# Optimization experiments

Measured on AMD Instinct MI355X. Metric: run time of the kernel, lower is better.

## Reference

```python
import jax, jax.numpy as jnp
import numpy as np

EPS = 1e-5
GROUPS = 32


def conv1x1(x, W, b):
    # x: (B,C,T), W: (O,C), b: (O,)
    return jnp.einsum('bct,oc->bot', x, W) + b[None, :, None]


def group_norm(x, gamma, beta):
    B, C, T = x.shape
    xg = x.reshape(B, GROUPS, (C // GROUPS) * T)
    mu = xg.mean(axis=-1, keepdims=True)
    var = xg.var(axis=-1, keepdims=True)
    xn = ((xg - mu) * jax.lax.rsqrt(var + EPS)).reshape(B, C, T)
    return xn * gamma[None, :, None] + beta[None, :, None]


def block(x, W, b, gamma, beta):
    return jax.nn.relu(group_norm(conv1x1(x, W, b), gamma, beta))


def setup_inputs() -> dict:
    key = jax.random.key(0)
    ks = jax.random.split(key, 8)
    B, C, P, T, TF = 4, 512, 512, 2048, 4096
    inp = {
        'feature': jax.random.normal(ks[0], (B, C, T), jnp.float32),
        'frame_level_feature': jax.random.uniform(ks[1], (B, C, TF), jnp.float32),
        # cur_point_conv: conv1x1 C->P + GN(32,P)
        'W1': jax.random.normal(ks[2], (P, C), jnp.float32) / np.sqrt(C),
        'b1': jnp.zeros((P,), jnp.float32),
        'g1': jnp.ones((P,), jnp.float32),
        'be1': jnp.zeros((P,), jnp.float32),
        # lr_conv: conv1x1 C->2P + GN(32,2P)
        'W2': jax.random.normal(ks[3], (2 * P, C), jnp.float32) / np.sqrt(C),
        'b2': jnp.zeros((2 * P,), jnp.float32),
        'g2': jnp.ones((2 * P,), jnp.float32),
        'be2': jnp.zeros((2 * P,), jnp.float32),
        # proposal_conv: conv1x1 4P->C + GN(32,C)
        'W3': jax.random.normal(ks[4], (C, 4 * P), jnp.float32) / np.sqrt(4 * P),
        'b3': jnp.zeros((C,), jnp.float32),
        'g3': jnp.ones((C,), jnp.float32),
        'be3': jnp.zeros((C,), jnp.float32),
    }
    return inp


def reference(feature, frame_level_feature, W1, b1, g1, be1, W2, b2, g2, be2, W3, b3, g3, be3):
    fm_short = block(feature, W1, b1, g1, be1)          # (B,P,T)
    feat = block(feature, W2, b2, g2, be2)              # (B,2P,T)
    t = feature.shape[2]
    # inverse-CDF resampling (uses batch 0 statistics, as original)
    mean_values = frame_level_feature.mean(axis=1)[0]   # (TF,)
    mean_values = mean_values / mean_values.sum()
    cdf = (jnp.cumsum(mean_values) * t).astype(jnp.int32)
    cdf = jnp.minimum(cdf, t - 1)                       # (TF,)
    # exact vectorization of findNearNum loop: first index with minimal |cdf-i|
    targets = jnp.arange(t, dtype=jnp.int32)
    idx = jnp.argmin(jnp.abs(cdf[None, :] - targets[:, None]), axis=1)  # (t,)
    sampled = frame_level_feature[:, :, idx]            # (B,C,t)
    mixed = jnp.concatenate([sampled, feat, fm_short], axis=1)  # (B,4P,t)
    mixed = block(mixed, W3, b3, g3, be3)               # (B,C,t)
    return (mixed, feat)
```

## Files before the change

### kernel.cpp

```cpp
#include <hip/hip_runtime.h>

typedef unsigned short u16;
typedef unsigned int   u32;
typedef __attribute__((ext_vector_type(8))) short short8;
typedef __attribute__((ext_vector_type(4))) float f32x4;

__device__ __forceinline__ float bf2f(u16 v) {
  return __uint_as_float(((u32)v) << 16);
}
__device__ __forceinline__ u16 f2bf(float f) {
  u32 u = __float_as_uint(f);
  u32 r = (u + 0x7FFFu + ((u >> 16) & 1u)) >> 16;
  return (u16)r;
}
__device__ __forceinline__ float relu(float x) { return x < 0.f ? 0.f : x; }

__device__ __forceinline__ void gld16(const void* g, void* l) {
  __builtin_amdgcn_global_load_lds((const __attribute__((address_space(1))) u32*)g,
                                   (__attribute__((address_space(3))) u32*)l, 16, 0, 0);
}

__global__ void colmean_part_kernel(const float* __restrict__ frame,
                                    double* __restrict__ partD) {
  int tf = blockIdx.x * 256 + threadIdx.x;
  int ch = blockIdx.y;
  const float* f0 = frame + tf + (size_t)ch * 64 * 4096;
  double s = 0.0;
  for (int c = 0; c < 64; ++c) s += (double)f0[(size_t)c * 4096];
  partD[ch * 4096 + tf] = s;
}

__global__ void scanD_kernel(const double* __restrict__ partD, int* __restrict__ cdf) {
  __shared__ double part[256];
  __shared__ double base[256];
  __shared__ double Ss;
  int tid = threadIdx.x;
  double loc[16];
  double s = 0.0;
#pragma unroll
  for (int i = 0; i < 16; ++i) {
    int tf = tid * 16 + i;
    double m = 0.0;
#pragma unroll
    for (int ch = 0; ch < 8; ++ch) m += partD[ch * 4096 + tf];
    loc[i] = m / 512.0;
    s += loc[i];
  }
  part[tid] = s;
  __syncthreads();
  if (tid == 0) {
    double t = 0.0;
    for (int i = 0; i < 256; ++i) t += part[i];
    Ss = t;
  }
  __syncthreads();
  double S = Ss;
  s = 0.0;
#pragma unroll
  for (int i = 0; i < 16; ++i) { loc[i] = loc[i] / S; s += loc[i]; }
  part[tid] = s;
  __syncthreads();
  if (tid == 0) {
    double c = 0.0;
    for (int i = 0; i < 256; ++i) { base[i] = c; c += part[i]; }
  }
  __syncthreads();
  double c = base[tid];
#pragma unroll
  for (int i = 0; i < 16; ++i) {
    c += loc[i];
    int iv = (int)(c * 2048.0);
    cdf[tid * 16 + i] = iv < 2047 ? iv : 2047;
  }
}

__global__ void argmin_kernel(const int* __restrict__ cdf, int* __restrict__ idx) {
  __shared__ int sd[256], sj[256];
  int target = blockIdx.x;
  int tid = threadIdx.x;
  int best = 0x7fffffff, bj = 0x7fffffff;
  for (int j = tid; j < 4096; j += 256) {
    int d = cdf[j] - target; d = d < 0 ? -d : d;
    if (d < best) { best = d; bj = j; }
  }
  sd[tid] = best; sj[tid] = bj;
  __syncthreads();
  for (int s = 128; s > 0; s >>= 1) {
    if (tid < s) {
      if (sd[tid+s] < sd[tid] || (sd[tid+s] == sd[tid] && sj[tid+s] < sj[tid])) {
        sd[tid] = sd[tid+s]; sj[tid] = sj[tid+s];
      }
    }
    __syncthreads();
  }
  if (tid == 0) idx[target] = sj[0];
}

__global__ void gatherT_kernel(const float* __restrict__ frame, const int* __restrict__ idx,
                               u16* __restrict__ X3T) {
  __shared__ u16 tile[64][65];
  __shared__ int sidx[64];
  int cb = blockIdx.x * 64, t0 = blockIdx.y * 64, b = blockIdx.z;
  int tid = threadIdx.x;
  if (tid < 64) {
    int it = idx[t0 + tid];
    sidx[tid] = it < 0 ? 0 : (it > 4095 ? 4095 : it);
  }
  __syncthreads();
  const float* fb = frame + (size_t)b * 512 * 4096;
  for (int i = tid; i < 4096; i += 256) {
    int r = i >> 6, tt = i & 63;
    tile[tt][r] = f2bf(fb[(size_t)(cb + r) * 4096 + sidx[tt]]);
  }
  __syncthreads();
  u16* xb = X3T + (size_t)b * 2048 * 2048;
  for (int i = tid; i < 4096; i += 256) {
    int r = i >> 6, cc = i & 63;
    xb[(size_t)(t0 + r) * 2048 + cb + cc] = tile[r][cc];
  }
}

__global__ void transposeCT_kernel(const float* __restrict__ X, u16* __restrict__ XT) {
  __shared__ u16 tile[64][65];
  int cb = blockIdx.x * 64, t0 = blockIdx.y * 64, b = blockIdx.z;
  int tid = threadIdx.x;
  const float* xb = X + (size_t)b * 512 * 2048;
  for (int i = tid; i < 4096; i += 256) {
    int r = i >> 6, tt = i & 63;
    tile[tt][r] = f2bf(xb[(size_t)(cb + r) * 2048 + t0 + tt]);
  }
  __syncthreads();
  u16* xtb = XT + (size_t)b * 2048 * 512;
  for (int i = tid; i < 4096; i += 256) {
    int r = i >> 6, cc = i & 63;
    xtb[(size_t)(t0 + r) * 512 + cb + cc] = tile[r][cc];
  }
}

__global__ void convW12_kernel(const float* __restrict__ W1, const float* __restrict__ W2,
                               u16* __restrict__ dst) {
  int i = blockIdx.x * 256 + threadIdx.x;
  dst[i] = f2bf(i < 262144 ? W1[i] : W2[i - 262144]);
}
__global__ void convW_kernel(const float* __restrict__ src, u16* __restrict__ dst, int n) {
  int i = blockIdx.x * 256 + threadIdx.x;
  if (i < n) dst[i] = f2bf(src[i]);
}

__global__ __launch_bounds__(128) void gemm12_kernel(
    const u16* __restrict__ A, const u16* __restrict__ Bt,
    const float* __restrict__ b1, const float* __restrict__ b2,
    float* __restrict__ Y)
{
  const int K = 512;
  __shared__ short As[2][2048];
  __shared__ short Bs[2][4096];
  const int tid = threadIdx.x;
  const int lane = tid & 63;
  const int w = tid >> 6;
  const int nt = blockIdx.x, mt = blockIdx.y, bb = blockIdx.z;
  const u16* Ab = A + (size_t)mt * 64 * K;
  const u16* Bb = Bt + ((size_t)bb * 2048 + (size_t)nt * 128) * K;
  const int lm = lane & 15, lq = lane >> 4;
  f32x4 acc[4][4] = {};

  auto stage = [&](int buf, int kt) {
#pragma unroll
    for (int p = 0; p < 2; ++p) {
      int chunk = tid + 128 * p;
      int row = chunk >> 2, ko = (chunk & 3) << 3;
      gld16(Ab + (size_t)row * K + kt + ko, (char*)As[buf] + chunk * 16);
    }
#pragma unroll
    for (int p = 0; p < 4; ++p) {
      int chunk = tid + 128 * p;
      int row = chunk >> 2, ko = (chunk & 3) << 3;
      gld16(Bb + (size_t)row * K + kt + ko, (char*)Bs[buf] + chunk * 16);
    }
  };

  stage(0, 0);
  for (int s = 0; s < 16; ++s) {
    int cur = s & 1;
    __syncthreads();
    if (s + 1 < 16) stage(cur ^ 1, (s + 1) << 5);
    short8 af[4], bfv[4];
#pragma unroll
    for (int i = 0; i < 4; ++i)
      af[i] = *(const short8*)(As[cur] + ((i * 16 + lm) * 32 + lq * 8));
#pragma unroll
    for (int j = 0; j < 4; ++j)
      bfv[j] = *(const short8*)(Bs[cur] + ((w * 64 + j * 16 + lm) * 32 + lq * 8));
#pragma unroll
    for (int i = 0; i < 4; ++i)
#pragma unroll
      for (int j = 0; j < 4; ++j)
        acc[i][j] = __builtin_amdgcn_mfma_f32_16x16x32_bf16(af[i], bfv[j], acc[i][j], 0, 0, 0);
  }
#pragma unroll
  for (int i = 0; i < 4; ++i) {
    int mbase = mt * 64 + i * 16 + lq * 4;
#pragma unroll
    for (int e = 0; e < 4; ++e) {
      int m = mbase + e;
      float bv = m < 512 ? b1[m] : b2[m - 512];
      float* yp = Y + ((size_t)bb * 1536 + m) * 2048 + nt * 128 + w * 64 + lm;
#pragma unroll
      for (int j = 0; j < 4; ++j)
        yp[j * 16] = acc[i][j][e] + bv;
    }
  }
}

__global__ __launch_bounds__(128) void gemm3s_kernel(
    const u16* __restrict__ A, const u16* __restrict__ Bt,
    const float* __restrict__ bias, float* __restrict__ Yp)
{
  const int K = 2048;
  __shared__ short As[2][2048];
  __shared__ short Bs[2][4096];
  const int tid = threadIdx.x;
  const int lane = tid & 63;
  const int w = tid >> 6;
  const int nt = blockIdx.x, mt = blockIdx.y;
  const int bb = blockIdx.z >> 1, ks = blockIdx.z & 1;
  const u16* Ab = A + (size_t)mt * 64 * K + ks * 1024;
  const u16* Bb = Bt + ((size_t)bb * 2048 + (size_t)nt * 128) * K + ks * 1024;
  const int lm = lane & 15, lq = lane >> 4;
  f32x4 acc[4][4] = {};

  auto stage = [&](int buf, int kt) {
#pragma unroll
    for (int p = 0; p < 2; ++p) {
      int chunk = tid + 128 * p;
      int row = chunk >> 2, ko = (chunk & 3) << 3;
      gld16(Ab + (size_t)row * K + kt + ko, (char*)As[buf] + chunk * 16);
    }
#pragma unroll
    for (int p = 0; p < 4; ++p) {
      int chunk = tid + 128 * p;
      int row = chunk >> 2, ko = (chunk & 3) << 3;
      gld16(Bb + (size_t)row * K + kt + ko, (char*)Bs[buf] + chunk * 16);
    }
  };

  stage(0, 0);
  for (int s = 0; s < 32; ++s) {
    int cur = s & 1;
    __syncthreads();
    if (s + 1 < 32) stage(cur ^ 1, (s + 1) << 5);
    short8 af[4], bfv[4];
#pragma unroll
    for (int i = 0; i < 4; ++i)
      af[i] = *(const short8*)(As[cur] + ((i * 16 + lm) * 32 + lq * 8));
#pragma unroll
    for (int j = 0; j < 4; ++j)
      bfv[j] = *(const short8*)(Bs[cur] + ((w * 64 + j * 16 + lm) * 32 + lq * 8));
#pragma unroll
    for (int i = 0; i < 4; ++i)
#pragma unroll
      for (int j = 0; j < 4; ++j)
        acc[i][j] = __builtin_amdgcn_mfma_f32_16x16x32_bf16(af[i], bfv[j], acc[i][j], 0, 0, 0);
  }
#pragma unroll
  for (int i = 0; i < 4; ++i) {
    int mbase = mt * 64 + i * 16 + lq * 4;
#pragma unroll
    for (int e = 0; e < 4; ++e) {
      int m = mbase + e;
      float bv = ks ? 0.f : bias[m];
      float* yp = Yp + ((size_t)(ks * 4 + bb) * 512 + m) * 2048 + nt * 128 + w * 64 + lm;
#pragma unroll
      for (int j = 0; j < 4; ++j)
        yp[j * 16] = acc[i][j][e] + bv;
    }
  }
}

__global__ void statsP12_kernel(const float* __restrict__ Y12,
                                float* __restrict__ raw1, float* __restrict__ raw2) {
  int chunk = blockIdx.x, gy = blockIdx.y, b = blockIdx.z, tid = threadIdx.x;
  int cpg, chBase, g; float* raw;
  if (gy < 32) { if (chunk >= 8) return; cpg = 16; chBase = 0;   g = gy;      raw = raw1; }
  else         {                         cpg = 32; chBase = 512; g = gy - 32; raw = raw2; }
  const float* base = Y12 + ((size_t)b * 1536 + chBase + g * cpg) * 2048 + (size_t)chunk * 4096;
  float s = 0.f, ss = 0.f;
#pragma unroll
  for (int i = 0; i < 16; ++i) { float v = base[tid + 256 * i]; s += v; ss += v * v; }
  __shared__ float s1[256], s2[256];
  s1[tid] = s; s2[tid] = ss;
  __syncthreads();
  for (int st = 128; st > 0; st >>= 1) {
    if (tid < st) { s1[tid] += s1[tid + st]; s2[tid] += s2[tid + st]; }
    __syncthreads();
  }
  if (tid == 0) {
    atomicAdd(&raw[(b * 32 + g) * 2],     s1[0]);
    atomicAdd(&raw[(b * 32 + g) * 2 + 1], s2[0]);
  }
}

__global__ void stats3p_kernel(const float* __restrict__ Yp, float* __restrict__ raw) {
  int chunk = blockIdx.x, g = blockIdx.y, b = blockIdx.z, tid = threadIdx.x;
  const float* base = Yp + ((size_t)b * 512 + g * 16) * 2048 + (size_t)chunk * 4096;
  float s = 0.f, ss = 0.f;
#pragma unroll
  for (int i = 0; i < 16; ++i) {
    int o = tid + 256 * i;
    float v = base[o] + base[o + 4194304];
    s += v; ss += v * v;
  }
  __shared__ float s1[256], s2[256];
  s1[tid] = s; s2[tid] = ss;
  __syncthreads();
  for (int st = 128; st > 0; st >>= 1) {
    if (tid < st) { s1[tid] += s1[tid + st]; s2[tid] += s2[tid + st]; }
    __syncthreads();
  }
  if (tid == 0) {
    atomicAdd(&raw[(b * 32 + g) * 2],     s1[0]);
    atomicAdd(&raw[(b * 32 + g) * 2 + 1], s2[0]);
  }
}

__global__ void statsFin12_kernel(const float* __restrict__ raw1, const float* __restrict__ raw2,
                                  float* __restrict__ st1, float* __restrict__ st2) {
  int i = threadIdx.x;
  const float* raw = i < 128 ? raw1 : raw2;
  float* st = i < 128 ? st1 : st2;
  int j = i & 127;
  float n = i < 128 ? 32768.f : 65536.f;
  float mu = raw[j * 2] / n;
  float var = raw[j * 2 + 1] / n - mu * mu;
  st[j * 2] = mu;
  st[j * 2 + 1] = 1.0f / sqrtf(var + 1e-5f);
}
__global__ void statsFin_kernel(const float* __restrict__ raw, float* __restrict__ stats,
                                float n) {
  int i = threadIdx.x;
  float mu = raw[i * 2] / n;
  float var = raw[i * 2 + 1] / n - mu * mu;
  stats[i * 2] = mu;
  stats[i * 2 + 1] = 1.0f / sqrtf(var + 1e-5f);
}

__global__ void normT_kernel(const float* __restrict__ Y, const float* __restrict__ stats,
                             const float* __restrict__ gamma, const float* __restrict__ beta,
                             int rowsB, int chBase, int C, int gShift,
                             u16* __restrict__ X3T, int colBase,
                             float* __restrict__ featOut) {
  __shared__ u16 tile[64][65];
  int b = blockIdx.z, c0 = blockIdx.y * 64, t0 = blockIdx.x * 64;
  const float* yb = Y + ((size_t)b * rowsB + chBase) * 2048;
  for (int i = threadIdx.x; i < 4096; i += 256) {
    int r = i >> 6, cc = i & 63;
    int ch = c0 + r;
    int gI = (b * 32 + (ch >> gShift)) * 2;
    float mu = stats[gI], rs = stats[gI + 1];
    float v = yb[(size_t)ch * 2048 + t0 + cc];
    float o = relu((v - mu) * rs * gamma[ch] + beta[ch]);
    tile[cc][r] = f2bf(o);
    if (featOut) featOut[((size_t)b * C + ch) * 2048 + t0 + cc] = o;
  }
  __syncthreads();
  for (int i = threadIdx.x; i < 4096; i += 256) {
    int r = i >> 6, cc = i & 63;
    X3T[((size_t)b * 2048 + t0 + r) * 2048 + colBase + c0 + cc] = tile[r][cc];
  }
}

__global__ void norm3_kernel(const float* __restrict__ Yp, const float* __restrict__ stats,
                             const float* __restrict__ gamma, const float* __restrict__ beta,
                             float* __restrict__ out) {
  int i = blockIdx.x * 256 + threadIdx.x;
  int b = i >> 20;
  int ch = (i >> 11) & 511;
  int gI = (b * 32 + (ch >> 4)) * 2;
  float mu = stats[gI], rs = stats[gI + 1];
  float v = Yp[i] + Yp[i + 4194304];
  out[i] = relu((v - mu) * rs * gamma[ch] + beta[ch]);
}

extern "C" void kernel_launch(void* const* d_in, const int* in_sizes, int n_in,
                              void* d_out, int out_size, void* d_ws, size_t ws_size,
                              hipStream_t stream) {
  const float* feature = (const float*)d_in[0];
  const float* frame   = (const float*)d_in[1];
  const float* W1 = (const float*)d_in[2];
  const float* b1 = (const float*)d_in[3];
  const float* g1 = (const float*)d_in[4];
  const float* be1 = (const float*)d_in[5];
  const float* W2 = (const float*)d_in[6];
  const float* b2 = (const float*)d_in[7];
  const float* g2 = (const float*)d_in[8];
  const float* be2 = (const float*)d_in[9];
  const float* W3 = (const float*)d_in[10];
  const float* b3 = (const float*)d_in[11];
  const float* g3 = (const float*)d_in[12];
  const float* be3 = (const float*)d_in[13];

  char* ws = (char*)d_ws;
  u16*    X3T   = (u16*)(ws + 0);
  float*  Y12f  = (float*)(ws + 33554432);
  float*  Y3p   = (float*)(ws + 33554432);
  u16*    W3b   = (u16*)(ws + 67108864);
  double* partD = (double*)(ws + 50331648);
  u16*    featT = (u16*)(ws + 83886080);
  u16*    W12b  = (u16*)(ws + 92274688);
  int*    cdf   = (int*)(ws + 93847552);
  int*    idx   = (int*)(ws + 93863936);
  float*  raw1  = (float*)(ws + 93872128);
  float*  raw2  = (float*)(ws + 93873152);
  float*  raw3  = (float*)(ws + 93874176);
  float*  st1   = (float*)(ws + 93875200);
  float*  st2   = (float*)(ws + 93876224);
  float*  st3   = (float*)(ws + 93877248);

  float* outMixed = (float*)d_out;
  float* outFeat  = outMixed + (size_t)4 * 512 * 2048;

  hipMemsetAsync(raw1, 0, 3 * 1024, stream);

  colmean_part_kernel<<<dim3(16, 8), 256, 0, stream>>>(frame, partD);
  scanD_kernel<<<1, 256, 0, stream>>>(partD, cdf);
  argmin_kernel<<<2048, 256, 0, stream>>>(cdf, idx);
  gatherT_kernel<<<dim3(8, 32, 4), 256, 0, stream>>>(frame, idx, X3T);
  transposeCT_kernel<<<dim3(8, 32, 4), 256, 0, stream>>>(feature, featT);

  convW12_kernel<<<3072, 256, 0, stream>>>(W1, W2, W12b);
  gemm12_kernel<<<dim3(16, 24, 4), 128, 0, stream>>>(W12b, featT, b1, b2, Y12f);
  statsP12_kernel<<<dim3(16, 64, 4), 256, 0, stream>>>(Y12f, raw1, raw2);
  statsFin12_kernel<<<1, 256, 0, stream>>>(raw1, raw2, st1, st2);
  normT_kernel<<<dim3(32, 8, 4), 256, 0, stream>>>(Y12f, st1, g1, be1, 1536, 0, 512, 4,
                                                   X3T, 1536, (float*)nullptr);
  normT_kernel<<<dim3(32, 16, 4), 256, 0, stream>>>(Y12f, st2, g2, be2, 1536, 512, 1024, 5,
                                                    X3T, 512, outFeat);
  convW_kernel<<<4096, 256, 0, stream>>>(W3, W3b, 1048576);
  gemm3s_kernel<<<dim3(16, 8, 8), 128, 0, stream>>>(W3b, X3T, b3, Y3p);
  stats3p_kernel<<<dim3(8, 32, 4), 256, 0, stream>>>(Y3p, raw3);
  statsFin_kernel<<<1, 128, 0, stream>>>(raw3, st3, 32768.f);
  norm3_kernel<<<16384, 256, 0, stream>>>(Y3p, st3, g3, be3, outMixed);
}
```

Baseline: 285.9 us.

## Enlarge GEMM tiles to 128x128, swizzle LDS, fuse GN stats into gemm12

Both GEMM kernels move to 256-thread blocks with 128x128 output tiles arranged as a 2x2 wave grid, which halves the number of M tiles and raises A/B reuse per block. LDS staging now XOR-swizzles the k-chunk offset by row to reduce bank conflicts on the fragment reads. gemm12 also accumulates per-group sum and sum-of-squares in its epilogue with wave shuffles and atomics, so the separate statsP12 pass that re-read Y12 is removed. The cost is fewer blocks in flight and higher register pressure, plus more atomic traffic and a change in floating-point summation order.

```diff
diff --git a/kernel.cpp b/kernel.cpp
--- a/kernel.cpp
+++ b/kernel.cpp
@@ -147,19 +147,20 @@
   if (i < n) dst[i] = f2bf(src[i]);
 }
 
-__global__ __launch_bounds__(128) void gemm12_kernel(
+__global__ __launch_bounds__(256) void gemm12_kernel(
     const u16* __restrict__ A, const u16* __restrict__ Bt,
     const float* __restrict__ b1, const float* __restrict__ b2,
-    float* __restrict__ Y)
+    float* __restrict__ Y, float* __restrict__ raw1, float* __restrict__ raw2)
 {
   const int K = 512;
-  __shared__ short As[2][2048];
+  __shared__ short As[2][4096];
   __shared__ short Bs[2][4096];
   const int tid = threadIdx.x;
   const int lane = tid & 63;
   const int w = tid >> 6;
+  const int wr = w >> 1, wc = w & 1;
   const int nt = blockIdx.x, mt = blockIdx.y, bb = blockIdx.z;
-  const u16* Ab = A + (size_t)mt * 64 * K;
+  const u16* Ab = A + (size_t)mt * 128 * K;
   const u16* Bb = Bt + ((size_t)bb * 2048 + (size_t)nt * 128) * K;
   const int lm = lane & 15, lq = lane >> 4;
   f32x4 acc[4][4] = {};
@@ -167,14 +168,16 @@
   auto stage = [&](int buf, int kt) {
 #pragma unroll
     for (int p = 0; p < 2; ++p) {
-      int chunk = tid + 128 * p;
-      int row = chunk >> 2, ko = (chunk & 3) << 3;
+      int chunk = tid + 256 * p;
+      int row = chunk >> 2;
+      int ko = ((chunk & 3) ^ ((row >> 1) & 3)) << 3;
       gld16(Ab + (size_t)row * K + kt + ko, (char*)As[buf] + chunk * 16);
     }
 #pragma unroll
-    for (int p = 0; p < 4; ++p) {
-      int chunk = tid + 128 * p;
-      int row = chunk >> 2, ko = (chunk & 3) << 3;
+    for (int p = 0; p < 2; ++p) {
+      int chunk = tid + 256 * p;
+      int row = chunk >> 2;
+      int ko = ((chunk & 3) ^ ((row >> 1) & 3)) << 3;
       gld16(Bb + (size_t)row * K + kt + ko, (char*)Bs[buf] + chunk * 16);
     }
   };
@@ -186,45 +189,81 @@
     if (s + 1 < 16) stage(cur ^ 1, (s + 1) << 5);
     short8 af[4], bfv[4];
 #pragma unroll
-    for (int i = 0; i < 4; ++i)
-      af[i] = *(const short8*)(As[cur] + ((i * 16 + lm) * 32 + lq * 8));
-#pragma unroll
-    for (int j = 0; j < 4; ++j)
-      bfv[j] = *(const short8*)(Bs[cur] + ((w * 64 + j * 16 + lm) * 32 + lq * 8));
+    for (int i = 0; i < 4; ++i) {
+      int r = wr * 64 + i * 16 + lm;
+      af[i] = *(const short8*)(As[cur] + r * 32 + ((lq ^ ((r >> 1) & 3)) << 3));
+    }
+#pragma unroll
+    for (int j = 0; j < 4; ++j) {
+      int r = wc * 64 + j * 16 + lm;
+      bfv[j] = *(const short8*)(Bs[cur] + r * 32 + ((lq ^ ((r >> 1) & 3)) << 3));
+    }
 #pragma unroll
     for (int i = 0; i < 4; ++i)
 #pragma unroll
       for (int j = 0; j < 4; ++j)
         acc[i][j] = __builtin_amdgcn_mfma_f32_16x16x32_bf16(af[i], bfv[j], acc[i][j], 0, 0, 0);
   }
+
+  float s1[4] = {0.f, 0.f, 0.f, 0.f};
+  float s2[4] = {0.f, 0.f, 0.f, 0.f};
 #pragma unroll
   for (int i = 0; i < 4; ++i) {
-    int mbase = mt * 64 + i * 16 + lq * 4;
+    int mbase = mt * 128 + wr * 64 + i * 16 + lq * 4;
 #pragma unroll
     for (int e = 0; e < 4; ++e) {
       int m = mbase + e;
       float bv = m < 512 ? b1[m] : b2[m - 512];
-      float* yp = Y + ((size_t)bb * 1536 + m) * 2048 + nt * 128 + w * 64 + lm;
-#pragma unroll
-      for (int j = 0; j < 4; ++j)
-        yp[j * 16] = acc[i][j][e] + bv;
-    }
-  }
-}
-
-__global__ __launch_bounds__(128) void gemm3s_kernel(
+      float* yp = Y + ((size_t)bb * 1536 + m) * 2048 + nt * 128 + wc * 64 + lm;
+#pragma unroll
+      for (int j = 0; j < 4; ++j) {
+        float v = acc[i][j][e] + bv;
+        yp[j * 16] = v;
+        s1[i] += v; s2[i] += v * v;
+      }
+    }
+  }
+#pragma unroll
+  for (int i = 0; i < 4; ++i) {
+#pragma unroll
+    for (int off = 32; off > 0; off >>= 1) {
+      s1[i] += __shfl_xor(s1[i], off);
+      s2[i] += __shfl_xor(s2[i], off);
+    }
+  }
+  if (lane == 0) {
+    if (mt < 4) {
+#pragma unroll
+      for (int i = 0; i < 4; ++i) {
+        int g = mt * 8 + wr * 4 + i;
+        atomicAdd(&raw1[(bb * 32 + g) * 2],     s1[i]);
+        atomicAdd(&raw1[(bb * 32 + g) * 2 + 1], s2[i]);
+      }
+    } else {
+#pragma unroll
+      for (int i = 0; i < 2; ++i) {
+        int g = (mt - 4) * 4 + wr * 2 + i;
+        atomicAdd(&raw2[(bb * 32 + g) * 2],     s1[2 * i] + s1[2 * i + 1]);
+        atomicAdd(&raw2[(bb * 32 + g) * 2 + 1], s2[2 * i] + s2[2 * i + 1]);
+      }
+    }
+  }
+}
+
+__global__ __launch_bounds__(256) void gemm3s_kernel(
     const u16* __restrict__ A, const u16* __restrict__ Bt,
     const float* __restrict__ bias, float* __restrict__ Yp)
 {
   const int K = 2048;
-  __shared__ short As[2][2048];
+  __shared__ short As[2][4096];
   __shared__ short Bs[2][4096];
   const int tid = threadIdx.x;
   const int lane = tid & 63;
   const int w = tid >> 6;
+  const int wr = w >> 1, wc = w & 1;
   const int nt = blockIdx.x, mt = blockIdx.y;
   const int bb = blockIdx.z >> 1, ks = blockIdx.z & 1;
-  const u16* Ab = A + (size_t)mt * 64 * K + ks * 1024;
+  const u16* Ab = A + (size_t)mt * 128 * K + ks * 1024;
   const u16* Bb = Bt + ((size_t)bb * 2048 + (size_t)nt * 128) * K + ks * 1024;
   const int lm = lane & 15, lq = lane >> 4;
   f32x4 acc[4][4] = {};
@@ -232,14 +271,16 @@
   auto stage = [&](int buf, int kt) {
 #pragma unroll
     for (int p = 0; p < 2; ++p) {
-      int chunk = tid + 128 * p;
-      int row = chunk >> 2, ko = (chunk & 3) << 3;
+      int chunk = tid + 256 * p;
+      int row = chunk >> 2;
+      int ko = ((chunk & 3) ^ ((row >> 1) & 3)) << 3;
       gld16(Ab + (size_t)row * K + kt + ko, (char*)As[buf] + chunk * 16);
     }
 #pragma unroll
-    for (int p = 0; p < 4; ++p) {
-      int chunk = tid + 128 * p;
-      int row = chunk >> 2, ko = (chunk & 3) << 3;
+    for (int p = 0; p < 2; ++p) {
+      int chunk = tid + 256 * p;
+      int row = chunk >> 2;
+      int ko = ((chunk & 3) ^ ((row >> 1) & 3)) << 3;
       gld16(Bb + (size_t)row * K + kt + ko, (char*)Bs[buf] + chunk * 16);
     }
   };
@@ -251,11 +292,15 @@
     if (s + 1 < 32) stage(cur ^ 1, (s + 1) << 5);
     short8 af[4], bfv[4];
 #pragma unroll
-    for (int i = 0; i < 4; ++i)
-      af[i] = *(const short8*)(As[cur] + ((i * 16 + lm) * 32 + lq * 8));
-#pragma unroll
-    for (int j = 0; j < 4; ++j)
-      bfv[j] = *(const short8*)(Bs[cur] + ((w * 64 + j * 16 + lm) * 32 + lq * 8));
+    for (int i = 0; i < 4; ++i) {
+      int r = wr * 64 + i * 16 + lm;
+      af[i] = *(const short8*)(As[cur] + r * 32 + ((lq ^ ((r >> 1) & 3)) << 3));
+    }
+#pragma unroll
+    for (int j = 0; j < 4; ++j) {
+      int r = wc * 64 + j * 16 + lm;
+      bfv[j] = *(const short8*)(Bs[cur] + r * 32 + ((lq ^ ((r >> 1) & 3)) << 3));
+    }
 #pragma unroll
     for (int i = 0; i < 4; ++i)
 #pragma unroll
@@ -264,39 +309,16 @@
   }
 #pragma unroll
   for (int i = 0; i < 4; ++i) {
-    int mbase = mt * 64 + i * 16 + lq * 4;
+    int mbase = mt * 128 + wr * 64 + i * 16 + lq * 4;
 #pragma unroll
     for (int e = 0; e < 4; ++e) {
       int m = mbase + e;
       float bv = ks ? 0.f : bias[m];
-      float* yp = Yp + ((size_t)(ks * 4 + bb) * 512 + m) * 2048 + nt * 128 + w * 64 + lm;
+      float* yp = Yp + ((size_t)(ks * 4 + bb) * 512 + m) * 2048 + nt * 128 + wc * 64 + lm;
 #pragma unroll
       for (int j = 0; j < 4; ++j)
         yp[j * 16] = acc[i][j][e] + bv;
     }
-  }
-}
-
-__global__ void statsP12_kernel(const float* __restrict__ Y12,
-                                float* __restrict__ raw1, float* __restrict__ raw2) {
-  int chunk = blockIdx.x, gy = blockIdx.y, b = blockIdx.z, tid = threadIdx.x;
-  int cpg, chBase, g; float* raw;
-  if (gy < 32) { if (chunk >= 8) return; cpg = 16; chBase = 0;   g = gy;      raw = raw1; }
-  else         {                         cpg = 32; chBase = 512; g = gy - 32; raw = raw2; }
-  const float* base = Y12 + ((size_t)b * 1536 + chBase + g * cpg) * 2048 + (size_t)chunk * 4096;
-  float s = 0.f, ss = 0.f;
-#pragma unroll
-  for (int i = 0; i < 16; ++i) { float v = base[tid + 256 * i]; s += v; ss += v * v; }
-  __shared__ float s1[256], s2[256];
-  s1[tid] = s; s2[tid] = ss;
-  __syncthreads();
-  for (int st = 128; st > 0; st >>= 1) {
-    if (tid < st) { s1[tid] += s1[tid + st]; s2[tid] += s2[tid + st]; }
-    __syncthreads();
-  }
-  if (tid == 0) {
-    atomicAdd(&raw[(b * 32 + g) * 2],     s1[0]);
-    atomicAdd(&raw[(b * 32 + g) * 2 + 1], s2[0]);
   }
 }
 
@@ -428,15 +450,15 @@
   transposeCT_kernel<<<dim3(8, 32, 4), 256, 0, stream>>>(feature, featT);
 
   convW12_kernel<<<3072, 256, 0, stream>>>(W1, W2, W12b);
-  gemm12_kernel<<<dim3(16, 24, 4), 128, 0, stream>>>(W12b, featT, b1, b2, Y12f);
-  statsP12_kernel<<<dim3(16, 64, 4), 256, 0, stream>>>(Y12f, raw1, raw2);
+  gemm12_kernel<<<dim3(16, 12, 4), 256, 0, stream>>>(W12b, featT, b1, b2, Y12f,
+                                                     raw1, raw2);
   statsFin12_kernel<<<1, 256, 0, stream>>>(raw1, raw2, st1, st2);
   normT_kernel<<<dim3(32, 8, 4), 256, 0, stream>>>(Y12f, st1, g1, be1, 1536, 0, 512, 4,
                                                    X3T, 1536, (float*)nullptr);
   normT_kernel<<<dim3(32, 16, 4), 256, 0, stream>>>(Y12f, st2, g2, be2, 1536, 512, 1024, 5,
                                                     X3T, 512, outFeat);
   convW_kernel<<<4096, 256, 0, stream>>>(W3, W3b, 1048576);
-  gemm3s_kernel<<<dim3(16, 8, 8), 128, 0, stream>>>(W3b, X3T, b3, Y3p);
+  gemm3s_kernel<<<dim3(16, 4, 8), 256, 0, stream>>>(W3b, X3T, b3, Y3p);
   stats3p_kernel<<<dim3(8, 32, 4), 256, 0, stream>>>(Y3p, raw3);
   statsFin_kernel<<<1, 128, 0, stream>>>(raw3, st3, 32768.f);
   norm3_kernel<<<16384, 256, 0, stream>>>(Y3p, st3, g3, be3, outMixed);
```

After: 285.1 us. Within noise of the previous version (-0.3%).
